# Kernel optimization log

Hardware: AMD Instinct MI355X
Metric: run time of the kernel (lower is better)

## Reference

```python
import jax, jax.numpy as jnp
from jax import lax
import numpy as np

EPS = 1e-3  # Keras BatchNormalization default epsilon

def cond_conv(x, experts, rw, rb):
    # x: [B,H,W,Cin]; experts: [E,kh,kw,Cin,Cout]
    pooled = jnp.mean(x, axis=(1, 2))                       # [B,Cin]
    route = jax.nn.sigmoid(pooled @ rw + rb)                # [B,E]
    kernels = jnp.einsum('be,ehwio->bhwio', route, experts) # per-example kernel
    def conv1(xi, ki):
        return lax.conv_general_dilated(
            xi[None], ki, window_strides=(1, 1), padding='SAME',
            dimension_numbers=('NHWC', 'HWIO', 'NHWC'))[0]
    return jax.vmap(conv1)(x, kernels)

def bn_inf(x, gamma, beta, mean, var):
    inv = gamma * lax.rsqrt(var + EPS)
    return x * inv + (beta - mean * inv)

def maxpool2(x):
    return lax.reduce_window(x, -jnp.inf, lax.max,
                             (1, 2, 2, 1), (1, 2, 2, 1), 'SAME')

def se_block(x, w1, w2):
    s = jnp.mean(x, axis=(1, 2))          # [B,C]
    s = jax.nn.relu(s @ w1)
    s = jax.nn.sigmoid(s @ w2)
    return x * s[:, None, None, :]

def setup_inputs() -> dict:
    key = jax.random.key(0)
    ks = jax.random.split(key, 12)
    d = {
        'x': jax.random.normal(ks[0], (64, 128, 128, 6), jnp.float32),
        'experts1': jax.random.normal(ks[1], (3, 3, 3, 6, 32), jnp.float32) * 0.1,
        'route1_w': jax.random.normal(ks[2], (6, 3), jnp.float32) * 0.1,
        'route1_b': jnp.zeros((3,), jnp.float32),
        'bn1_gamma': jnp.ones((32,), jnp.float32), 'bn1_beta': jnp.zeros((32,), jnp.float32),
        'bn1_mean': jnp.zeros((32,), jnp.float32), 'bn1_var': jnp.ones((32,), jnp.float32),
        'se1_w1': jax.random.normal(ks[3], (32, 2), jnp.float32) * 0.1,
        'se1_w2': jax.random.normal(ks[4], (2, 32), jnp.float32) * 0.1,
        'experts2': jax.random.normal(ks[5], (3, 3, 3, 32, 64), jnp.float32) * 0.05,
        'route2_w': jax.random.normal(ks[6], (32, 3), jnp.float32) * 0.1,
        'route2_b': jnp.zeros((3,), jnp.float32),
        'bn2_gamma': jnp.ones((64,), jnp.float32), 'bn2_beta': jnp.zeros((64,), jnp.float32),
        'bn2_mean': jnp.zeros((64,), jnp.float32), 'bn2_var': jnp.ones((64,), jnp.float32),
        'se2_w1': jax.random.normal(ks[7], (64, 4), jnp.float32) * 0.1,
        'se2_w2': jax.random.normal(ks[8], (4, 64), jnp.float32) * 0.1,
        'experts3': jax.random.normal(ks[9], (3, 3, 3, 64, 128), jnp.float32) * 0.05,
        'route3_w': jax.random.normal(ks[10], (64, 3), jnp.float32) * 0.1,
        'route3_b': jnp.zeros((3,), jnp.float32),
        'bn3_gamma': jnp.ones((128,), jnp.float32), 'bn3_beta': jnp.zeros((128,), jnp.float32),
        'bn3_mean': jnp.zeros((128,), jnp.float32), 'bn3_var': jnp.ones((128,), jnp.float32),
    }
    return d

def reference(x, experts1, route1_w, route1_b, bn1_gamma, bn1_beta, bn1_mean, bn1_var,
              se1_w1, se1_w2, experts2, route2_w, route2_b, bn2_gamma, bn2_beta,
              bn2_mean, bn2_var, se2_w1, se2_w2, experts3, route3_w, route3_b,
              bn3_gamma, bn3_beta, bn3_mean, bn3_var):
    h = cond_conv(x, experts1, route1_w, route1_b)
    h = jax.nn.relu(bn_inf(h, bn1_gamma, bn1_beta, bn1_mean, bn1_var))
    h = maxpool2(h)                       # [B,64,64,32]
    h = se_block(h, se1_w1, se1_w2)
    h = cond_conv(h, experts2, route2_w, route2_b)
    h = jax.nn.relu(bn_inf(h, bn2_gamma, bn2_beta, bn2_mean, bn2_var))
    h = maxpool2(h)                       # [B,32,32,64]
    h = se_block(h, se2_w1, se2_w2)
    h = cond_conv(h, experts3, route3_w, route3_b)
    h = bn_inf(h, bn3_gamma, bn3_beta, bn3_mean, bn3_var)
    return jnp.mean(h, axis=(1, 2))       # [B,128]
```

## Files before the change

### kernel.cpp

```cpp
#include <hip/hip_runtime.h>

#define EPSBN 1e-3f

typedef unsigned short ushort_t;
typedef __attribute__((ext_vector_type(8))) short bf8;
typedef __attribute__((ext_vector_type(4))) float f4;

__device__ __forceinline__ float sigmoidf_(float z) {
  return 1.0f / (1.0f + expf(-z));
}

__device__ __forceinline__ ushort_t f2bf(float x) {
  union { float f; unsigned u; } v; v.f = x;
  unsigned r = (v.u + 0x7fffu + ((v.u >> 16) & 1u)) >> 16;
  return (ushort_t)r;
}

__device__ __forceinline__ float bfbits2f(unsigned hi_bits) {
  union { unsigned u; float f; } v; v.u = hi_bits;
  return v.f;
}

__global__ void k_mean_x(const float* __restrict__ x, float* __restrict__ part) {
  const int b = blockIdx.x >> 2;
  const int q = blockIdx.x & 3;
  const int tid = threadIdx.x;
  float acc[6] = {0.f, 0.f, 0.f, 0.f, 0.f, 0.f};
  const float* xb = x + (size_t)b * (128 * 128 * 6);
  for (int i = 0; i < 16; ++i) {
    const int p = q * 4096 + i * 256 + tid;
    const float* px = xb + (size_t)p * 6;
#pragma unroll
    for (int c = 0; c < 6; ++c) acc[c] += px[c];
  }
#pragma unroll
  for (int c = 0; c < 6; ++c)
    for (int off = 32; off > 0; off >>= 1) acc[c] += __shfl_down(acc[c], off, 64);
  __shared__ float red[4][6];
  const int lane = tid & 63, w = tid >> 6;
  if (lane == 0) {
#pragma unroll
    for (int c = 0; c < 6; ++c) red[w][c] = acc[c];
  }
  __syncthreads();
  if (tid < 6) {
    part[blockIdx.x * 6 + tid] = red[0][tid] + red[1][tid] + red[2][tid] + red[3][tid];
  }
}

__global__ void k_buildk1(const float* __restrict__ part,
                          const float* __restrict__ experts1,
                          const float* __restrict__ rw, const float* __restrict__ rb,
                          const float* __restrict__ gamma, const float* __restrict__ var,
                          ushort_t* __restrict__ k1b) {
  const int b = blockIdx.x;
  const int tid = threadIdx.x;
  __shared__ float route[3];
  if (tid < 3) {
    float z = rb[tid];
    for (int c = 0; c < 6; ++c) {
      const float s = part[(b * 4 + 0) * 6 + c] + part[(b * 4 + 1) * 6 + c] +
                      part[(b * 4 + 2) * 6 + c] + part[(b * 4 + 3) * 6 + c];
      z += (s * (1.0f / 16384.0f)) * rw[c * 3 + tid];
    }
    route[tid] = sigmoidf_(z);
  }
  __syncthreads();
  const float r0 = route[0], r1 = route[1], r2 = route[2];
  for (int s = tid; s < 3072; s += 256) {
    const int j = s & 7;
    const int lane = (s >> 3) & 63;
    const int nt = (s >> 9) & 1;
    const int ky = s >> 10;
    const int lx = lane & 15, lg = lane >> 4;
    const int co = nt * 16 + lx;
    float val = 0.f;
    if (lg < 3 && j < 6) {
      const int idx = ((ky * 3 + lg) * 6 + j) * 32 + co;
      const float v = r0 * experts1[idx] + r1 * experts1[1728 + idx] + r2 * experts1[3456 + idx];
      val = v * gamma[co] * rsqrtf(var[co] + EPSBN);
    }
    k1b[(size_t)b * 3072 + s] = f2bf(val);
  }
}

__global__ __launch_bounds__(256)
void k_conv1(const float* __restrict__ x, const ushort_t* __restrict__ k1b,
             const float* __restrict__ gamma, const float* __restrict__ beta,
             const float* __restrict__ bnmean, const float* __restrict__ bnvar,
             ushort_t* __restrict__ p1b) {
  const int bid = blockIdx.x;
  const int b = bid >> 3;
  const int tyi = (bid >> 1) & 3;
  const int txi = bid & 1;
  __shared__ __align__(16) ushort_t patch[34 * 68 * 8];
  const int tid = threadIdx.x;
  const float* xb = x + (size_t)b * (128 * 128 * 6);

  for (int v = tid; v < 34 * 68; v += 256) {
    const int ry = v / 68, p = v - ry * 68;
    const int gy = tyi * 32 - 1 + ry, gx = txi * 64 - 1 + p;
    uint4 u = make_uint4(0u, 0u, 0u, 0u);
    if (((unsigned)gy < 128u) && ((unsigned)gx < 128u)) {
      const float* s = xb + ((size_t)(gy * 128 + gx)) * 6;
      const float2 a0 = *(const float2*)s;
      const float2 a1 = *(const float2*)(s + 2);
      const float2 a2 = *(const float2*)(s + 4);
      u.x = (unsigned)f2bf(a0.x) | ((unsigned)f2bf(a0.y) << 16);
      u.y = (unsigned)f2bf(a1.x) | ((unsigned)f2bf(a1.y) << 16);
      u.z = (unsigned)f2bf(a2.x) | ((unsigned)f2bf(a2.y) << 16);
      u.w = 0u;
    }
    *(uint4*)(patch + (size_t)v * 8) = u;
  }

  const int w = tid >> 6;
  const int lane = tid & 63;
  const int lx = lane & 15, lg = lane >> 4;

  bf8 Bf[3][2];
#pragma unroll
  for (int ky = 0; ky < 3; ++ky)
#pragma unroll
    for (int nt = 0; nt < 2; ++nt)
      Bf[ky][nt] = *(const bf8*)(k1b + (size_t)b * 3072 + ((size_t)((ky * 2 + nt) * 64 + lane)) * 8);

  const int co0 = lx, co1 = 16 + lx;
  const float inv0 = gamma[co0] * rsqrtf(bnvar[co0] + EPSBN);
  const float bias0 = beta[co0] - bnmean[co0] * inv0;
  const float inv1 = gamma[co1] * rsqrtf(bnvar[co1] + EPSBN);
  const float bias1 = beta[co1] - bnmean[co1] * inv1;

  __syncthreads();

#pragma unroll
  for (int rp = 0; rp < 4; ++rp) {
    const int y0 = w * 8 + rp * 2;
    const int prow = tyi * 16 + w * 4 + rp;
#pragma unroll
    for (int xt = 0; xt < 4; ++xt) {
      bf8 Af[4];
#pragma unroll
      for (int ri = 0; ri < 4; ++ri)
        Af[ri] = *(const bf8*)(patch + ((size_t)(y0 + ri) * 68 + xt * 16 + lx + lg) * 8);
      f4 acc0[2], acc1[2];
#pragma unroll
      for (int nt = 0; nt < 2; ++nt) {
        acc0[nt] = (f4){0.f, 0.f, 0.f, 0.f};
        acc1[nt] = (f4){0.f, 0.f, 0.f, 0.f};
      }
#pragma unroll
      for (int ky = 0; ky < 3; ++ky) {
#pragma unroll
        for (int nt = 0; nt < 2; ++nt) {
          acc0[nt] = __builtin_amdgcn_mfma_f32_16x16x32_bf16(Af[ky], Bf[ky][nt], acc0[nt], 0, 0, 0);
          acc1[nt] = __builtin_amdgcn_mfma_f32_16x16x32_bf16(Af[ky + 1], Bf[ky][nt], acc1[nt], 0, 0, 0);
        }
      }
#pragma unroll
      for (int nt = 0; nt < 2; ++nt) {
        const float inv = nt ? inv1 : inv0;
        const float bias = nt ? bias1 : bias0;
        const int co = nt * 16 + lx;
#pragma unroll
        for (int q = 0; q < 2; ++q) {
          const float m0 = fmaxf(acc0[nt][2 * q] + bias, 0.f);
          const float m1 = fmaxf(acc0[nt][2 * q + 1] + bias, 0.f);
          const float m2 = fmaxf(acc1[nt][2 * q] + bias, 0.f);
          const float m3 = fmaxf(acc1[nt][2 * q + 1] + bias, 0.f);
          const float mx = fmaxf(fmaxf(m0, m1), fmaxf(m2, m3));
          const int pcol = txi * 32 + xt * 8 + lg * 2 + q;
          p1b[(((size_t)b * 64 + prow) * 64 + pcol) * 32 + co] = f2bf(mx);
        }
      }
    }
  }
}

__global__ void k_mean1(const ushort_t* __restrict__ p1b, float* __restrict__ part) {
  const int b = blockIdx.x >> 2;
  const int q = blockIdx.x & 3;
  const int tid = threadIdx.x;
  const int oct = tid & 3, row0 = tid >> 2;
  const ushort_t* base = p1b + (size_t)b * 131072;
  float s[8] = {0.f, 0.f, 0.f, 0.f, 0.f, 0.f, 0.f, 0.f};
  for (int k = 0; k < 16; ++k) {
    const int pos = q * 1024 + (k << 6) + row0;
    const uint4 u = *(const uint4*)(base + (size_t)pos * 32 + oct * 8);
    const unsigned uu[4] = {u.x, u.y, u.z, u.w};
#pragma unroll
    for (int j = 0; j < 4; ++j) {
      s[2 * j]     += bfbits2f(uu[j] << 16);
      s[2 * j + 1] += bfbits2f(uu[j] & 0xffff0000u);
    }
  }
  __shared__ float red[256][8];
#pragma unroll
  for (int j = 0; j < 8; ++j) red[tid][j] = s[j];
  __syncthreads();
  if (tid < 32) {
    float t = 0.f;
    const int o = tid >> 3, j = tid & 7;
    for (int r = 0; r < 64; ++r) t += red[r * 4 + o][j];
    part[blockIdx.x * 32 + tid] = t;
  }
}

__global__ void k_buildk2(const float* __restrict__ part,
                          const float* __restrict__ experts2,
                          const float* __restrict__ rw, const float* __restrict__ rb,
                          const float* __restrict__ w1, const float* __restrict__ w2,
                          const float* __restrict__ gamma, const float* __restrict__ var,
                          ushort_t* __restrict__ k2pb) {
  const int b = blockIdx.x, tid = threadIdx.x;
  __shared__ float m1[32], h[2], s1[32], route[3];
  if (tid < 32) {
    const float s = part[(b * 4 + 0) * 32 + tid] + part[(b * 4 + 1) * 32 + tid] +
                    part[(b * 4 + 2) * 32 + tid] + part[(b * 4 + 3) * 32 + tid];
    m1[tid] = s * (1.0f / 4096.0f);
  }
  __syncthreads();
  if (tid < 2) {
    float z = 0.f;
    for (int c = 0; c < 32; ++c) z += m1[c] * w1[c * 2 + tid];
    h[tid] = fmaxf(z, 0.f);
  }
  __syncthreads();
  if (tid < 32) s1[tid] = sigmoidf_(h[0] * w2[tid] + h[1] * w2[32 + tid]);
  __syncthreads();
  if (tid < 3) {
    float z = rb[tid];
    for (int c = 0; c < 32; ++c) z += m1[c] * s1[c] * rw[c * 3 + tid];
    route[tid] = sigmoidf_(z);
  }
  __syncthreads();
  const float r0 = route[0], r1 = route[1], r2 = route[2];
  for (int t = tid; t < 18432; t += 256) {
    const int co = t & 63;
    const int ci = (t >> 6) & 31;
    const int tap = t >> 11;
    const float inv = gamma[co] * rsqrtf(var[co] + EPSBN);
    const float v = r0 * experts2[t] + r1 * experts2[18432 + t] + r2 * experts2[2 * 18432 + t];
    k2pb[(size_t)b * 18432 + ((size_t)tap * 64 + co) * 32 + ci] = f2bf(v * s1[ci] * inv);
  }
}

__global__ __launch_bounds__(256)
void k_conv2(const ushort_t* __restrict__ p1b, const ushort_t* __restrict__ k2pb,
             const float* __restrict__ gamma, const float* __restrict__ beta,
             const float* __restrict__ bnmean, const float* __restrict__ bnvar,
             float* __restrict__ p2) {
  const int bi = blockIdx.x;
  const int b = bi >> 5;
  const int tile = (bi >> 1) & 15;
  const int cog = bi & 1;
  const int ty = tile >> 2, tx = tile & 3;
  __shared__ __align__(16) short smem[24480];
  short* As = smem;
  short* Bs = smem + 12960;
  const int tid = threadIdx.x;

  const ushort_t* pb = p1b + (size_t)b * 131072;
  for (int v = tid; v < 1296; v += 256) {
    const int cell = v >> 2, part = v & 3;
    const int ly = cell / 18, lx2 = cell - ly * 18;
    const int gy = ty * 16 - 1 + ly, gx = tx * 16 - 1 + lx2;
    uint4 d = make_uint4(0u, 0u, 0u, 0u);
    if (((unsigned)gy < 64u) && ((unsigned)gx < 64u))
      d = *(const uint4*)(pb + (((size_t)gy << 6) + gx) * 32 + part * 8);
    *(uint4*)(As + (ly * 18 + lx2) * 40 + part * 8) = d;
  }
  for (int v = tid; v < 1152; v += 256) {
    const int r = v >> 2, part = v & 3;
    const int t = r >> 5, n = r & 31;
    const uint4 d = *(const uint4*)(k2pb + (size_t)b * 18432 +
                                    ((size_t)(t * 64 + cog * 32 + n)) * 32 + part * 8);
    *(uint4*)(Bs + r * 40 + part * 8) = d;
  }
  __syncthreads();

  const int w = tid >> 6;
  const int lane = tid & 63;
  const int lx = lane & 15, lg = lane >> 4;

  f4 acc[4][2];
#pragma unroll
  for (int mt = 0; mt < 4; ++mt)
#pragma unroll
    for (int nt = 0; nt < 2; ++nt)
      acc[mt][nt] = (f4){0.f, 0.f, 0.f, 0.f};

#pragma unroll
  for (int t = 0; t < 9; ++t) {
    const int ky = t / 3, kx = t - 3 * (t / 3);
    bf8 Bf0 = *(const bf8*)(Bs + ((t << 5) + lx) * 40 + (lg << 3));
    bf8 Bf1 = *(const bf8*)(Bs + ((t << 5) + 16 + lx) * 40 + (lg << 3));
#pragma unroll
    for (int mt = 0; mt < 4; ++mt) {
      const int y = 4 * w + mt + ky;
      const bf8 Af = *(const bf8*)(As + (y * 18 + lx + kx) * 40 + (lg << 3));
      acc[mt][0] = __builtin_amdgcn_mfma_f32_16x16x32_bf16(Af, Bf0, acc[mt][0], 0, 0, 0);
      acc[mt][1] = __builtin_amdgcn_mfma_f32_16x16x32_bf16(Af, Bf1, acc[mt][1], 0, 0, 0);
    }
  }

#pragma unroll
  for (int nt = 0; nt < 2; ++nt) {
    const int co = cog * 32 + nt * 16 + lx;
    const float inv = gamma[co] * rsqrtf(bnvar[co] + EPSBN);
    const float bias = beta[co] - bnmean[co] * inv;
#pragma unroll
    for (int half = 0; half < 2; ++half) {
      const int prow = ty * 8 + 2 * w + half;
#pragma unroll
      for (int q = 0; q < 2; ++q) {
        const float m0 = fmaxf(acc[2 * half][nt][2 * q] + bias, 0.f);
        const float m1 = fmaxf(acc[2 * half][nt][2 * q + 1] + bias, 0.f);
        const float m2 = fmaxf(acc[2 * half + 1][nt][2 * q] + bias, 0.f);
        const float m3 = fmaxf(acc[2 * half + 1][nt][2 * q + 1] + bias, 0.f);
        const float mx = fmaxf(fmaxf(m0, m1), fmaxf(m2, m3));
        p2[(((size_t)b * 64 + co) * 32 + prow) * 32 + tx * 8 + 2 * lg + q] = mx;
      }
    }
  }
}

__global__ void k_s3(const float* __restrict__ p2, float* __restrict__ S_raw) {
  const int b = blockIdx.x >> 4, cb = blockIdx.x & 15;
  const int w = threadIdx.x >> 6, lane = threadIdx.x & 63;
  const int ci = cb * 4 + w;
  const float* plane = p2 + ((size_t)b * 64 + ci) * 1024;
  float t = 0.f, r0 = 0.f, rl = 0.f, c0 = 0.f, cl = 0.f;
  float k00 = 0.f, k01 = 0.f, k10 = 0.f, k11 = 0.f;
  const int c = lane & 31;
#pragma unroll
  for (int i = 0; i < 16; ++i) {
    const int idx = i * 64 + lane;
    const float v = plane[idx];
    const int r = idx >> 5;
    t += v;
    if (r == 0) r0 += v;
    if (r == 31) rl += v;
    if (c == 0) c0 += v;
    if (c == 31) cl += v;
    if (r == 0 && c == 0) k00 = v;
    if (r == 0 && c == 31) k01 = v;
    if (r == 31 && c == 0) k10 = v;
    if (r == 31 && c == 31) k11 = v;
  }
  for (int off = 32; off > 0; off >>= 1) {
    t += __shfl_down(t, off, 64);
    r0 += __shfl_down(r0, off, 64);
    rl += __shfl_down(rl, off, 64);
    c0 += __shfl_down(c0, off, 64);
    cl += __shfl_down(cl, off, 64);
    k00 += __shfl_down(k00, off, 64);
    k01 += __shfl_down(k01, off, 64);
    k10 += __shfl_down(k10, off, 64);
    k11 += __shfl_down(k11, off, 64);
  }
  if (lane == 0) {
    const float A[3] = {rl, 0.f, r0};
    const float B[3] = {cl, 0.f, c0};
    const float AB[3][3] = {{k11, 0.f, k10}, {0.f, 0.f, 0.f}, {k01, 0.f, k00}};
#pragma unroll
    for (int ky = 0; ky < 3; ++ky)
#pragma unroll
      for (int kx = 0; kx < 3; ++kx)
        S_raw[((size_t)b * 9 + ky * 3 + kx) * 64 + ci] = t - A[ky] - B[kx] + AB[ky][kx];
  }
}

__global__ void k_final(const float* __restrict__ S_raw, const float* __restrict__ experts3,
                        const float* __restrict__ rw, const float* __restrict__ rb,
                        const float* __restrict__ w1, const float* __restrict__ w2,
                        const float* __restrict__ gamma, const float* __restrict__ beta,
                        const float* __restrict__ bnmean, const float* __restrict__ bnvar,
                        float* __restrict__ out) {
  const int b = blockIdx.x;
  const int tid = threadIdx.x;
  __shared__ float m2[64], h[4], s2[64], route[3], Sp[9][64], redf[2][128];
  if (tid < 64) m2[tid] = S_raw[((size_t)b * 9 + 4) * 64 + tid] * (1.0f / 1024.0f);
  __syncthreads();
  if (tid < 4) {
    float z = 0.f;
    for (int c = 0; c < 64; ++c) z += m2[c] * w1[c * 4 + tid];
    h[tid] = fmaxf(z, 0.f);
  }
  __syncthreads();
  if (tid < 64) {
    float z = 0.f;
#pragma unroll
    for (int j = 0; j < 4; ++j) z += h[j] * w2[j * 64 + tid];
    s2[tid] = sigmoidf_(z);
  }
  __syncthreads();
  if (tid < 3) {
    float z = rb[tid];
    for (int c = 0; c < 64; ++c) z += m2[c] * s2[c] * rw[c * 3 + tid];
    route[tid] = sigmoidf_(z);
  }
  __syncthreads();
  for (int v = tid; v < 576; v += 256) {
    const int tap = v >> 6, ci = v & 63;
    Sp[tap][ci] = S_raw[((size_t)b * 9 + tap) * 64 + ci] * s2[ci];
  }
  __syncthreads();

  const int co = tid & 127;
  const int hf = tid >> 7;
  const int tap_lo = hf ? 5 : 0;
  const int tap_hi = hf ? 9 : 5;
  float acc = 0.f;
#pragma unroll
  for (int e = 0; e < 3; ++e) {
    float m = 0.f;
    for (int tap = tap_lo; tap < tap_hi; ++tap) {
      const float* E = experts3 + ((size_t)(e * 9 + tap) * 64) * 128 + co;
#pragma unroll 16
      for (int ci = 0; ci < 64; ++ci) m = fmaf(E[(size_t)ci * 128], Sp[tap][ci], m);
    }
    acc += route[e] * m;
  }
  redf[hf][co] = acc;
  __syncthreads();
  if (tid < 128) {
    const float total = redf[0][tid] + redf[1][tid];
    const float inv = gamma[tid] * rsqrtf(bnvar[tid] + EPSBN);
    out[(size_t)b * 128 + tid] = total * (1.0f / 1024.0f) * inv + (beta[tid] - bnmean[tid] * inv);
  }
}

extern "C" void kernel_launch(void* const* d_in, const int* in_sizes, int n_in,
                              void* d_out, int out_size, void* d_ws, size_t ws_size,
                              hipStream_t stream) {
  const float* x        = (const float*)d_in[0];
  const float* experts1 = (const float*)d_in[1];
  const float* rw1      = (const float*)d_in[2];
  const float* rb1      = (const float*)d_in[3];
  const float* g1  = (const float*)d_in[4];
  const float* be1 = (const float*)d_in[5];
  const float* mu1 = (const float*)d_in[6];
  const float* va1 = (const float*)d_in[7];
  const float* sw1a = (const float*)d_in[8];
  const float* sw1b = (const float*)d_in[9];
  const float* experts2 = (const float*)d_in[10];
  const float* rw2 = (const float*)d_in[11];
  const float* rb2 = (const float*)d_in[12];
  const float* g2  = (const float*)d_in[13];
  const float* be2 = (const float*)d_in[14];
  const float* mu2 = (const float*)d_in[15];
  const float* va2 = (const float*)d_in[16];
  const float* sw2a = (const float*)d_in[17];
  const float* sw2b = (const float*)d_in[18];
  const float* experts3 = (const float*)d_in[19];
  const float* rw3 = (const float*)d_in[20];
  const float* rb3 = (const float*)d_in[21];
  const float* g3  = (const float*)d_in[22];
  const float* be3 = (const float*)d_in[23];
  const float* mu3 = (const float*)d_in[24];
  const float* va3 = (const float*)d_in[25];
  float* out = (float*)d_out;
  float* ws = (float*)d_ws;

  float* meanx_part = ws;
  float* mean1_part = ws + 1536;
  ushort_t* k1b     = (ushort_t*)(ws + 9728);
  ushort_t* k2pb    = (ushort_t*)(ws + 108032);
  float* S_raw      = ws + 697856;
  ushort_t* p1b     = (ushort_t*)(ws + 734720);
  float* p2         = ws + 4929024;

  hipLaunchKernelGGL(k_mean_x, dim3(256), dim3(256), 0, stream, x, meanx_part);
  hipLaunchKernelGGL(k_buildk1, dim3(64), dim3(256), 0, stream,
                     meanx_part, experts1, rw1, rb1, g1, va1, k1b);
  hipLaunchKernelGGL(k_conv1, dim3(512), dim3(256), 0, stream,
                     x, k1b, g1, be1, mu1, va1, p1b);
  hipLaunchKernelGGL(k_mean1, dim3(256), dim3(256), 0, stream, p1b, mean1_part);
  hipLaunchKernelGGL(k_buildk2, dim3(64), dim3(256), 0, stream,
                     mean1_part, experts2, rw2, rb2, sw1a, sw1b, g2, va2, k2pb);
  hipLaunchKernelGGL(k_conv2, dim3(2048), dim3(256), 0, stream,
                     p1b, k2pb, g2, be2, mu2, va2, p2);
  hipLaunchKernelGGL(k_s3, dim3(1024), dim3(256), 0, stream, p2, S_raw);
  hipLaunchKernelGGL(k_final, dim3(64), dim3(256), 0, stream,
                     S_raw, experts3, rw3, rb3, sw2a, sw2b, g3, be3, mu3, va3, out);
}
```

Before: 221.8 us.

## Fuse channel means into conv epilogues and drop mean/s3 kernels

The first conv now reduces per-channel sums of its pooled output in-register and writes per-block partials, so the separate mean pass over p1b goes away. The second conv accumulates the nine border-masked tap sums directly in its epilogue instead of writing the full p2 tensor for a separate reduction kernel. This removes two kernel launches and a large intermediate write and read. In exchange it adds shuffle and shared-memory reductions in the conv epilogues, and the final kernel now sums partials with 512 threads split four ways over taps.

```diff
diff --git a/kernel.cpp b/kernel.cpp
--- a/kernel.cpp
+++ b/kernel.cpp
@@ -14,11 +14,6 @@
   union { float f; unsigned u; } v; v.f = x;
   unsigned r = (v.u + 0x7fffu + ((v.u >> 16) & 1u)) >> 16;
   return (ushort_t)r;
-}
-
-__device__ __forceinline__ float bfbits2f(unsigned hi_bits) {
-  union { unsigned u; float f; } v; v.u = hi_bits;
-  return v.f;
 }
 
 __global__ void k_mean_x(const float* __restrict__ x, float* __restrict__ part) {
@@ -88,12 +83,13 @@
 void k_conv1(const float* __restrict__ x, const ushort_t* __restrict__ k1b,
              const float* __restrict__ gamma, const float* __restrict__ beta,
              const float* __restrict__ bnmean, const float* __restrict__ bnvar,
-             ushort_t* __restrict__ p1b) {
+             ushort_t* __restrict__ p1b, float* __restrict__ part_m1) {
   const int bid = blockIdx.x;
   const int b = bid >> 3;
   const int tyi = (bid >> 1) & 3;
   const int txi = bid & 1;
   __shared__ __align__(16) ushort_t patch[34 * 68 * 8];
+  __shared__ float mred[4][32];
   const int tid = threadIdx.x;
   const float* xb = x + (size_t)b * (128 * 128 * 6);
 
@@ -133,6 +129,8 @@
 
   __syncthreads();
 
+  float msum0 = 0.f, msum1 = 0.f;
+
 #pragma unroll
   for (int rp = 0; rp < 4; ++rp) {
     const int y0 = w * 8 + rp * 2;
@@ -169,44 +167,30 @@
           const float m2 = fmaxf(acc1[nt][2 * q] + bias, 0.f);
           const float m3 = fmaxf(acc1[nt][2 * q + 1] + bias, 0.f);
           const float mx = fmaxf(fmaxf(m0, m1), fmaxf(m2, m3));
+          if (nt) msum1 += mx; else msum0 += mx;
           const int pcol = txi * 32 + xt * 8 + lg * 2 + q;
           p1b[(((size_t)b * 64 + prow) * 64 + pcol) * 32 + co] = f2bf(mx);
         }
       }
     }
   }
-}
-
-__global__ void k_mean1(const ushort_t* __restrict__ p1b, float* __restrict__ part) {
-  const int b = blockIdx.x >> 2;
-  const int q = blockIdx.x & 3;
-  const int tid = threadIdx.x;
-  const int oct = tid & 3, row0 = tid >> 2;
-  const ushort_t* base = p1b + (size_t)b * 131072;
-  float s[8] = {0.f, 0.f, 0.f, 0.f, 0.f, 0.f, 0.f, 0.f};
-  for (int k = 0; k < 16; ++k) {
-    const int pos = q * 1024 + (k << 6) + row0;
-    const uint4 u = *(const uint4*)(base + (size_t)pos * 32 + oct * 8);
-    const unsigned uu[4] = {u.x, u.y, u.z, u.w};
-#pragma unroll
-    for (int j = 0; j < 4; ++j) {
-      s[2 * j]     += bfbits2f(uu[j] << 16);
-      s[2 * j + 1] += bfbits2f(uu[j] & 0xffff0000u);
-    }
-  }
-  __shared__ float red[256][8];
-#pragma unroll
-  for (int j = 0; j < 8; ++j) red[tid][j] = s[j];
+
+  msum0 += __shfl_xor(msum0, 16, 64);
+  msum0 += __shfl_xor(msum0, 32, 64);
+  msum1 += __shfl_xor(msum1, 16, 64);
+  msum1 += __shfl_xor(msum1, 32, 64);
+  if (lg == 0) {
+    mred[w][lx] = msum0;
+    mred[w][16 + lx] = msum1;
+  }
   __syncthreads();
   if (tid < 32) {
-    float t = 0.f;
-    const int o = tid >> 3, j = tid & 7;
-    for (int r = 0; r < 64; ++r) t += red[r * 4 + o][j];
-    part[blockIdx.x * 32 + tid] = t;
-  }
-}
-
-__global__ void k_buildk2(const float* __restrict__ part,
+    part_m1[(size_t)bid * 32 + tid] =
+        mred[0][tid] + mred[1][tid] + mred[2][tid] + mred[3][tid];
+  }
+}
+
+__global__ void k_buildk2(const float* __restrict__ part_m1,
                           const float* __restrict__ experts2,
                           const float* __restrict__ rw, const float* __restrict__ rb,
                           const float* __restrict__ w1, const float* __restrict__ w2,
@@ -215,8 +199,9 @@
   const int b = blockIdx.x, tid = threadIdx.x;
   __shared__ float m1[32], h[2], s1[32], route[3];
   if (tid < 32) {
-    const float s = part[(b * 4 + 0) * 32 + tid] + part[(b * 4 + 1) * 32 + tid] +
-                    part[(b * 4 + 2) * 32 + tid] + part[(b * 4 + 3) * 32 + tid];
+    float s = 0.f;
+#pragma unroll
+    for (int k = 0; k < 8; ++k) s += part_m1[(size_t)(b * 8 + k) * 32 + tid];
     m1[tid] = s * (1.0f / 4096.0f);
   }
   __syncthreads();
@@ -249,13 +234,14 @@
 void k_conv2(const ushort_t* __restrict__ p1b, const ushort_t* __restrict__ k2pb,
              const float* __restrict__ gamma, const float* __restrict__ beta,
              const float* __restrict__ bnmean, const float* __restrict__ bnvar,
-             float* __restrict__ p2) {
+             float* __restrict__ part_s3) {
   const int bi = blockIdx.x;
   const int b = bi >> 5;
   const int tile = (bi >> 1) & 15;
   const int cog = bi & 1;
   const int ty = tile >> 2, tx = tile & 3;
   __shared__ __align__(16) short smem[24480];
+  __shared__ float sred[4][2][16][9];
   short* As = smem;
   short* Bs = smem + 12960;
   const int tid = threadIdx.x;
@@ -304,83 +290,90 @@
     }
   }
 
-#pragma unroll
-  for (int nt = 0; nt < 2; ++nt) {
-    const int co = cog * 32 + nt * 16 + lx;
-    const float inv = gamma[co] * rsqrtf(bnvar[co] + EPSBN);
-    const float bias = beta[co] - bnmean[co] * inv;
-#pragma unroll
-    for (int half = 0; half < 2; ++half) {
-      const int prow = ty * 8 + 2 * w + half;
-#pragma unroll
-      for (int q = 0; q < 2; ++q) {
+  float s3[2][9];
+#pragma unroll
+  for (int nt = 0; nt < 2; ++nt)
+#pragma unroll
+    for (int t = 0; t < 9; ++t) s3[nt][t] = 0.f;
+
+#pragma unroll
+  for (int half = 0; half < 2; ++half) {
+    const int prow = ty * 8 + 2 * w + half;
+    const bool rok0 = (prow < 31), rok2 = (prow > 0);
+#pragma unroll
+    for (int q = 0; q < 2; ++q) {
+      const int pcol = tx * 8 + 2 * lg + q;
+      const bool cok0 = (pcol < 31), cok2 = (pcol > 0);
+      const bool rok[3] = {rok0, true, rok2};
+      const bool cok[3] = {cok0, true, cok2};
+#pragma unroll
+      for (int nt = 0; nt < 2; ++nt) {
+        const int co = cog * 32 + nt * 16 + lx;
+        const float inv = gamma[co] * rsqrtf(bnvar[co] + EPSBN);
+        const float bias = beta[co] - bnmean[co] * inv;
         const float m0 = fmaxf(acc[2 * half][nt][2 * q] + bias, 0.f);
         const float m1 = fmaxf(acc[2 * half][nt][2 * q + 1] + bias, 0.f);
         const float m2 = fmaxf(acc[2 * half + 1][nt][2 * q] + bias, 0.f);
         const float m3 = fmaxf(acc[2 * half + 1][nt][2 * q + 1] + bias, 0.f);
         const float mx = fmaxf(fmaxf(m0, m1), fmaxf(m2, m3));
-        p2[(((size_t)b * 64 + co) * 32 + prow) * 32 + tx * 8 + 2 * lg + q] = mx;
+#pragma unroll
+        for (int ky = 0; ky < 3; ++ky)
+#pragma unroll
+          for (int kx = 0; kx < 3; ++kx)
+            if (rok[ky] && cok[kx]) s3[nt][ky * 3 + kx] += mx;
       }
     }
   }
-}
-
-__global__ void k_s3(const float* __restrict__ p2, float* __restrict__ S_raw) {
-  const int b = blockIdx.x >> 4, cb = blockIdx.x & 15;
-  const int w = threadIdx.x >> 6, lane = threadIdx.x & 63;
-  const int ci = cb * 4 + w;
-  const float* plane = p2 + ((size_t)b * 64 + ci) * 1024;
-  float t = 0.f, r0 = 0.f, rl = 0.f, c0 = 0.f, cl = 0.f;
-  float k00 = 0.f, k01 = 0.f, k10 = 0.f, k11 = 0.f;
-  const int c = lane & 31;
-#pragma unroll
-  for (int i = 0; i < 16; ++i) {
-    const int idx = i * 64 + lane;
-    const float v = plane[idx];
-    const int r = idx >> 5;
-    t += v;
-    if (r == 0) r0 += v;
-    if (r == 31) rl += v;
-    if (c == 0) c0 += v;
-    if (c == 31) cl += v;
-    if (r == 0 && c == 0) k00 = v;
-    if (r == 0 && c == 31) k01 = v;
-    if (r == 31 && c == 0) k10 = v;
-    if (r == 31 && c == 31) k11 = v;
-  }
-  for (int off = 32; off > 0; off >>= 1) {
-    t += __shfl_down(t, off, 64);
-    r0 += __shfl_down(r0, off, 64);
-    rl += __shfl_down(rl, off, 64);
-    c0 += __shfl_down(c0, off, 64);
-    cl += __shfl_down(cl, off, 64);
-    k00 += __shfl_down(k00, off, 64);
-    k01 += __shfl_down(k01, off, 64);
-    k10 += __shfl_down(k10, off, 64);
-    k11 += __shfl_down(k11, off, 64);
-  }
-  if (lane == 0) {
-    const float A[3] = {rl, 0.f, r0};
-    const float B[3] = {cl, 0.f, c0};
-    const float AB[3][3] = {{k11, 0.f, k10}, {0.f, 0.f, 0.f}, {k01, 0.f, k00}};
-#pragma unroll
-    for (int ky = 0; ky < 3; ++ky)
-#pragma unroll
-      for (int kx = 0; kx < 3; ++kx)
-        S_raw[((size_t)b * 9 + ky * 3 + kx) * 64 + ci] = t - A[ky] - B[kx] + AB[ky][kx];
-  }
-}
-
-__global__ void k_final(const float* __restrict__ S_raw, const float* __restrict__ experts3,
-                        const float* __restrict__ rw, const float* __restrict__ rb,
-                        const float* __restrict__ w1, const float* __restrict__ w2,
-                        const float* __restrict__ gamma, const float* __restrict__ beta,
-                        const float* __restrict__ bnmean, const float* __restrict__ bnvar,
-                        float* __restrict__ out) {
+
+#pragma unroll
+  for (int nt = 0; nt < 2; ++nt)
+#pragma unroll
+    for (int t = 0; t < 9; ++t) {
+      float v = s3[nt][t];
+      v += __shfl_xor(v, 16, 64);
+      v += __shfl_xor(v, 32, 64);
+      s3[nt][t] = v;
+    }
+  __syncthreads();
+  if (lg == 0) {
+#pragma unroll
+    for (int nt = 0; nt < 2; ++nt)
+#pragma unroll
+      for (int t = 0; t < 9; ++t) sred[w][nt][lx][t] = s3[nt][t];
+  }
+  __syncthreads();
+  for (int v = tid; v < 288; v += 256) {
+    const int tap = v >> 5;
+    const int colocal = v & 31;
+    const int nt = colocal >> 4, lxx = colocal & 15;
+    part_s3[(size_t)bi * 288 + v] =
+        sred[0][nt][lxx][tap] + sred[1][nt][lxx][tap] +
+        sred[2][nt][lxx][tap] + sred[3][nt][lxx][tap];
+  }
+}
+
+__global__ __launch_bounds__(512)
+void k_final(const float* __restrict__ part_s3, const float* __restrict__ experts3,
+             const float* __restrict__ rw, const float* __restrict__ rb,
+             const float* __restrict__ w1, const float* __restrict__ w2,
+             const float* __restrict__ gamma, const float* __restrict__ beta,
+             const float* __restrict__ bnmean, const float* __restrict__ bnvar,
+             float* __restrict__ out) {
   const int b = blockIdx.x;
   const int tid = threadIdx.x;
-  __shared__ float m2[64], h[4], s2[64], route[3], Sp[9][64], redf[2][128];
-  if (tid < 64) m2[tid] = S_raw[((size_t)b * 9 + 4) * 64 + tid] * (1.0f / 1024.0f);
+  __shared__ float S_loc[9][64], Sp[9][64], m2[64], h[4], s2[64], route[3], redf[4][128];
+
+  for (int v = tid; v < 576; v += 512) {
+    const int tap = v >> 6, ci = v & 63;
+    const int cg = ci >> 5, colocal = ci & 31;
+    float s = 0.f;
+#pragma unroll
+    for (int tile = 0; tile < 16; ++tile)
+      s += part_s3[(size_t)((b * 16 + tile) * 2 + cg) * 288 + tap * 32 + colocal];
+    S_loc[tap][ci] = s;
+  }
+  __syncthreads();
+  if (tid < 64) m2[tid] = S_loc[4][tid] * (1.0f / 1024.0f);
   __syncthreads();
   if (tid < 4) {
     float z = 0.f;
@@ -401,16 +394,16 @@
     route[tid] = sigmoidf_(z);
   }
   __syncthreads();
-  for (int v = tid; v < 576; v += 256) {
+  for (int v = tid; v < 576; v += 512) {
     const int tap = v >> 6, ci = v & 63;
-    Sp[tap][ci] = S_raw[((size_t)b * 9 + tap) * 64 + ci] * s2[ci];
+    Sp[tap][ci] = S_loc[tap][ci] * s2[ci];
   }
   __syncthreads();
 
   const int co = tid & 127;
-  const int hf = tid >> 7;
-  const int tap_lo = hf ? 5 : 0;
-  const int tap_hi = hf ? 9 : 5;
+  const int quarter = tid >> 7;
+  const int tap_lo = (quarter == 0) ? 0 : (2 * quarter + 1);
+  const int tap_hi = tap_lo + ((quarter == 0) ? 3 : 2);
   float acc = 0.f;
 #pragma unroll
   for (int e = 0; e < 3; ++e) {
@@ -422,10 +415,10 @@
     }
     acc += route[e] * m;
   }
-  redf[hf][co] = acc;
+  redf[quarter][co] = acc;
   __syncthreads();
   if (tid < 128) {
-    const float total = redf[0][tid] + redf[1][tid];
+    const float total = redf[0][tid] + redf[1][tid] + redf[2][tid] + redf[3][tid];
     const float inv = gamma[tid] * rsqrtf(bnvar[tid] + EPSBN);
     out[(size_t)b * 128 + tid] = total * (1.0f / 1024.0f) * inv + (beta[tid] - bnmean[tid] * inv);
   }
@@ -464,24 +457,21 @@
   float* ws = (float*)d_ws;
 
   float* meanx_part = ws;
-  float* mean1_part = ws + 1536;
-  ushort_t* k1b     = (ushort_t*)(ws + 9728);
-  ushort_t* k2pb    = (ushort_t*)(ws + 108032);
-  float* S_raw      = ws + 697856;
-  ushort_t* p1b     = (ushort_t*)(ws + 734720);
-  float* p2         = ws + 4929024;
+  float* part_m1    = ws + 1536;
+  ushort_t* k1b     = (ushort_t*)(ws + 17920);
+  ushort_t* k2pb    = (ushort_t*)(ws + 116224);
+  float* part_s3    = ws + 706048;
+  ushort_t* p1b     = (ushort_t*)(ws + 1295872);
 
   hipLaunchKernelGGL(k_mean_x, dim3(256), dim3(256), 0, stream, x, meanx_part);
   hipLaunchKernelGGL(k_buildk1, dim3(64), dim3(256), 0, stream,
                      meanx_part, experts1, rw1, rb1, g1, va1, k1b);
   hipLaunchKernelGGL(k_conv1, dim3(512), dim3(256), 0, stream,
-                     x, k1b, g1, be1, mu1, va1, p1b);
-  hipLaunchKernelGGL(k_mean1, dim3(256), dim3(256), 0, stream, p1b, mean1_part);
+                     x, k1b, g1, be1, mu1, va1, p1b, part_m1);
   hipLaunchKernelGGL(k_buildk2, dim3(64), dim3(256), 0, stream,
-                     mean1_part, experts2, rw2, rb2, sw1a, sw1b, g2, va2, k2pb);
+                     part_m1, experts2, rw2, rb2, sw1a, sw1b, g2, va2, k2pb);
   hipLaunchKernelGGL(k_conv2, dim3(2048), dim3(256), 0, stream,
-                     p1b, k2pb, g2, be2, mu2, va2, p2);
-  hipLaunchKernelGGL(k_s3, dim3(1024), dim3(256), 0, stream, p2, S_raw);
-  hipLaunchKernelGGL(k_final, dim3(64), dim3(256), 0, stream,
-                     S_raw, experts3, rw3, rb3, sw2a, sw2b, g3, be3, mu3, va3, out);
-}
+                     p1b, k2pb, g2, be2, mu2, va2, part_s3);
+  hipLaunchKernelGGL(k_final, dim3(64), dim3(512), 0, stream,
+                     part_s3, experts3, rw3, rb3, sw2a, sw2b, g3, be3, mu3, va3, out);
+}
```

Result: faster. 207.3 us (-6.5%).
